# Optimization experiments

Hardware: AMD Instinct MI355X
Metric: run time of the kernel (lower is better)

Reference implementation:

```python
import jax, jax.numpy as jnp
import numpy as np

V0, V1, V2 = 8000, 4000, 4096   # diag / proc / med vocab sizes
E = 512                          # emb_dim
T, L = 64, 48                    # visits, codes per visit
FAI = 0.05                       # history-selection threshold
EPS = 1e-5                       # LayerNorm eps (torch default)

def _normalize(adj):
    # GCN.normalize: row-normalize (adj + I)
    adj = adj + np.eye(adj.shape[0], dtype=np.float64)
    rowsum = adj.sum(1)
    r_inv = np.where(rowsum > 0, 1.0 / rowsum, 0.0)
    return (r_inv[:, None] * adj).astype(np.float32)

def setup_inputs() -> dict:
    key = jax.random.key(0)
    ks = iter(jax.random.split(key, 48))
    p = lambda *s: jax.random.normal(next(ks), s, jnp.float32) * 0.02
    rng = np.random.default_rng(0)
    def rand_adj():
        a = rng.random((V2, V2)) < 0.01
        a = (a | a.T).astype(np.float64)
        np.fill_diagonal(a, 0.0)
        return a
    ehr = rand_adj(); ddi = rand_adj()
    return dict(
        diag_codes=jax.random.randint(next(ks), (T, L), 0, V0),
        proc_codes=jax.random.randint(next(ks), (T, L), 0, V1),
        emb0=p(V0, E), emb1=p(V1, E), emb2=p(V2, E),
        gru1_Wih=p(3 * E, E), gru1_Whh=p(3 * E, E), gru1_bih=p(3 * E), gru1_bhh=p(3 * E),
        gru2_Wih=p(3 * E, E), gru2_Whh=p(3 * E, E), gru2_bih=p(3 * E), gru2_bhh=p(3 * E),
        query_W=p(E, 2 * E), query_b=p(E),
        poly_h1_W=p(32, 2 * E), poly_h1_b=p(32), poly_gate_W=p(1, 32), poly_gate_b=p(1),
        cls_W=p(V2, 2 * E), cls_b=p(V2),
        ln_gamma=jnp.ones((E,), jnp.float32), ln_beta=jnp.zeros((E,), jnp.float32),
        ehr_W1=p(V2, E), ehr_b1=p(E), ehr_W2=p(E, E), ehr_b2=p(E),
        ddi_W1=p(V2, E), ddi_b1=p(E), ddi_W2=p(E, E), ddi_b2=p(E),
        inter1=p(1),
        ehr_adj_norm=jnp.asarray(_normalize(ehr)),
        ddi_adj_norm=jnp.asarray(_normalize(ddi)),
        ddi_adj=jnp.asarray(ddi.astype(np.float32)),
    )

def _gru_last(x_seq, mask, Wih, Whh, bih, bhh):
    # torch nn.GRU cell, batch=1; masked-out steps carry h unchanged, which
    # equals running the GRU over only the selected subsequence. Only the
    # final hidden state is needed (original uses output[-1]).
    def step(h, inp):
        x, m = inp
        gi = x @ Wih.T + bih          # [3E]
        gh = h @ Whh.T + bhh
        ir, iz, inn = jnp.split(gi, 3)
        hr, hz, hn = jnp.split(gh, 3)
        r = jax.nn.sigmoid(ir + hr)
        z = jax.nn.sigmoid(iz + hz)
        n = jnp.tanh(inn + r * hn)
        h_new = (1.0 - z) * n + z * h
        return jnp.where(m, h_new, h), None
    h0 = jnp.zeros((Wih.shape[1],), x_seq.dtype)
    h_final, _ = jax.lax.scan(step, h0, (x_seq, mask))
    return h_final

def reference(diag_codes, proc_codes, emb0, emb1, emb2,
              gru1_Wih, gru1_Whh, gru1_bih, gru1_bhh,
              gru2_Wih, gru2_Whh, gru2_bih, gru2_bhh,
              query_W, query_b, poly_h1_W, poly_h1_b, poly_gate_W, poly_gate_b,
              cls_W, cls_b, ln_gamma, ln_beta,
              ehr_W1, ehr_b1, ehr_W2, ehr_b2, ddi_W1, ddi_b1, ddi_W2, ddi_b2,
              inter1, ehr_adj_norm, ddi_adj_norm, ddi_adj):
    i1 = emb0[diag_codes].sum(1)            # [T,E] per-visit sum pooling
    i2 = emb1[proc_codes].sum(1)            # [T,E]
    rep = jnp.concatenate([i1, i2], -1)     # [T,2E] patient representation
    # Aggregation gate for history selection
    hidden = jax.nn.relu(rep @ poly_h1_W.T + poly_h1_b)
    gate = jax.nn.sigmoid(hidden @ poly_gate_W.T + poly_gate_b)[:, 0]  # [T]
    s = jnp.abs(gate[-1] - gate[:-1])
    mask = jnp.concatenate([s <= FAI, jnp.ones((1,), bool)])  # last visit always kept
    h1 = _gru_last(i1, mask, gru1_Wih, gru1_Whh, gru1_bih, gru1_bhh)
    h2 = _gru_last(i2, mask, gru2_Wih, gru2_Whh, gru2_bih, gru2_bhh)
    q_in = jnp.concatenate([h1, h2])                      # [2E]
    query = (jax.nn.relu(q_in) @ query_W.T + query_b)[None, :]  # [1,E]
    def gcn(W1, b1, W2, b2, adj):
        h = jax.nn.relu(adj @ W1 + b1)    # x = I so x@W1 = W1 (dropout eval)
        return adj @ (h @ W2) + b2
    safe = gcn(ehr_W1, ehr_b1, ehr_W2, ehr_b2, ehr_adj_norm) \
         - inter1 * gcn(ddi_W1, ddi_b1, ddi_W2, ddi_b2, ddi_adj_norm)
    drug = safe + emb2                                    # [V2,E]
    kw = jax.nn.softmax(query @ drug.T, -1)               # [1,V2]
    med = kw @ drug                                       # [1,E]
    mu = query.mean(-1, keepdims=True)
    var = ((query - mu) ** 2).mean(-1, keepdims=True)
    ln = (query - mu) / jnp.sqrt(var + EPS) * ln_gamma + ln_beta
    final = jnp.concatenate([ln, med], -1)                # [1,2E]
    result = jax.nn.relu(final) @ cls_W.T + cls_b         # [1,V2]
    neg = jax.nn.sigmoid(result)
    batch_neg = 0.0005 * ((neg.T * neg) * ddi_adj).sum()
    return result, batch_neg
```

## Files before the change

### kernel.cpp

```cpp
#include <hip/hip_runtime.h>
#include <cstdint>
#include <cstddef>

typedef unsigned short u16;
typedef unsigned int   u32;

typedef __bf16 bf16x8 __attribute__((ext_vector_type(8)));
typedef float  f32x4  __attribute__((ext_vector_type(4)));

__device__ __forceinline__ float uAsF(u32 u){ union{u32 u; float f;} c; c.u=u; return c.f; }
__device__ __forceinline__ float b2f(u16 v){ return uAsF(((u32)v)<<16); }
__device__ __forceinline__ u16 f2b(float f){
  union{float f; u32 u;} c; c.f=f; u32 x=c.u;
  u32 r = (x + 0x7fffu + ((x>>16)&1u)) >> 16;
  return (u16)r;
}
__device__ __forceinline__ void unpack8(uint4 p, float* f){
  f[0]=uAsF(p.x<<16); f[1]=uAsF(p.x&0xffff0000u);
  f[2]=uAsF(p.y<<16); f[3]=uAsF(p.y&0xffff0000u);
  f[4]=uAsF(p.z<<16); f[5]=uAsF(p.z&0xffff0000u);
  f[6]=uAsF(p.w<<16); f[7]=uAsF(p.w&0xffff0000u);
}
__device__ __forceinline__ float sigm(float x){ return 1.f/(1.f+__expf(-x)); }

// ... 180 lines not shown
      og[(size_t)(t0+2)*1536 + j] = a2 + b;
      og[(size_t)(t0+3)*1536 + j] = a3 + b;
      __syncthreads();
      if (tid == 0){
        __threadfence();
        __hip_atomic_fetch_add(&bars[31], 1u, __ATOMIC_RELAXED, __HIP_MEMORY_SCOPE_AGENT);
      }
      return;
    }
    rb -= 96;
    if (rb < 2048 + nt2){
      const void* S = (rb < 2048) ? trS : trS2;
      u16* D = (rb < 2048) ? trD : trD2;
      int t = (rb < 2048) ? rb : rb - 2048;
      __shared__ u16 tile[32][33];
      int bx = t & 15, by = t >> 4;
      int lx = tid & 31, ly = tid >> 5;
      int c = bx*32 + lx;
      #pragma unroll
      for (int i=0;i<2;i++){
        int r = by*32 + ly + i*16;
        size_t idx = (size_t)r*512 + c;
        tile[ly+i*16][lx] = f32 ? f2b(((const float*)S)[idx]) : ((const u16*)S)[idx];
      }
      __syncthreads();
      int r2 = by*32 + lx;
      #pragma unroll
      for (int i=0;i<2;i++){
        int c2 = bx*32 + ly + i*16;
        D[(size_t)c2*4096 + r2] = tile[lx][ly+i*16];
      }
      return;
    }
    rb -= 2048 + nt2;
    if (rb < nc0){
      size_t i8 = ((size_t)rb*512 + tid)*8;
      *(uint4*)(cv0D + i8) = ld8p(cv0S, i8, f32);
      return;
    }
    rb -= nc0;
    if (rb < nc1){
      size_t i8 = ((size_t)rb*512 + tid)*8;
      *(uint4*)(cv1D + i8) = ld8p(cv1S, i8, f32);
      return;
    }
    return;
  }

  const int b = blockIdx.x;
  const int g = b >> 3;
  const int w = b & 7;
  const int e0 = w * 64;
  const void* Whh = g ? Whh1 : Whh0;
  const void* bhh = g ? bhh1 : bhh0;
  const float* gig = gi + (size_t)g*64*1536;

  const int rg = tid & 31;
  const int cg = tid >> 5;

  __shared__ float h_lds[512];
  __shared__ float part[192*17];
  __shared__ float gh_l[192];
  __shared__ float gl[64];
  __shared__ int   mask_l[64];

  u32 wreg[96];
  #pragma unroll
  for (int i=0;i<6;i++){
    int lr = rg*6 + i;
    int grow = (lr >> 6)*512 + e0 + (lr & 63);
    size_t base = (size_t)grow*512 + cg*32;
    if (f32){
      const float2* src = (const float2*)((const float*)Whh + base);
      #pragma unroll
      for (int q=0;q<16;q++){
        float2 v = src[q];
        wreg[i*16+q] = (u32)f2b(v.x) | ((u32)f2b(v.y)<<16);
      }
    } else {
      const uint4* src = (const uint4*)((const u16*)Whh + base);
      #pragma unroll
      for (int q=0;q<4;q++){
        uint4 pk = src[q];
        wreg[i*16+q*4+0]=pk.x; wreg[i*16+q*4+1]=pk.y;
        wreg[i*16+q*4+2]=pk.z; wreg[i*16+q*4+3]=pk.w;
      }
    }
  }
  if (tid < 64) gl[tid] = gate[tid];
  h_lds[tid] = 0.f;
  __syncthreads();
  if (tid < 64)
    mask_l[tid] = (tid==63) ? 1 : (fabsf(gl[63] - gl[tid]) <= 0.05f ? 1 : 0);
  __syncthreads();
  if (tid == 0){
    while (__hip_atomic_load(&bars[31], __ATOMIC_RELAXED, __HIP_MEMORY_SCOPE_AGENT) < 96u)
      __builtin_amdgcn_s_sleep(2);
    __threadfence();
  }
  __syncthreads();

  int s = 0;
  for (int t=0;t<64;t++){
    if (!mask_l[t]) continue;
    s++;
    const int p = s & 1;
    float acc6[6] = {0.f,0.f,0.f,0.f,0.f,0.f};
    const float2* h2 = ((const float2*)h_lds) + cg*16;
    #pragma unroll
    for (int q=0;q<16;q++){
      float2 hv = h2[q];
      #pragma unroll
      for (int i=0;i<6;i++){
        u32 wp = wreg[i*16+q];
        acc6[i] += uAsF(wp<<16)*hv.x + uAsF(wp&0xffff0000u)*hv.y;
      }
    }
    #pragma unroll
    for (int i=0;i<6;i++) part[(rg*6+i)*17 + cg] = acc6[i];
    __syncthreads();
    if (tid < 192){
      const float* pp = part + tid*17;
      float ss = 0.f;
      #pragma unroll
      for (int q=0;q<16;q++) ss += pp[q];
      gh_l[tid] = ss;
    }
    __syncthreads();
    if (tid < 64){
      int e = e0 + tid;
      float hr = gh_l[tid]     + ld1(bhh, e, f32);
      float hz = gh_l[64+tid]  + ld1(bhh, 512+e, f32);
      float hn = gh_l[128+tid] + ld1(bhh, 1024+e, f32);
      const float* git = gig + (size_t)t*1536;
      float ir = git[e], iz = git[512+e], inn = git[1024+e];
      float r = sigm(ir + hr);
      float z = sigm(iz + hz);
      float n = tanhf(inn + r*hn);
      float hnew = (1.f - z)*n + z*h_lds[e];
      u32 word = ((u32)f2b(hnew) << 16) | (u32)s;
      __hip_atomic_store(hbuf + (size_t)p*1024 + g*512 + e, word,
                         __ATOMIC_RELAXED, __HIP_MEMORY_SCOPE_AGENT);
    }
    __syncthreads();
    {
      u32* src = hbuf + (size_t)p*1024 + g*512 + tid;
      u32 word = __hip_atomic_load(src, __ATOMIC_RELAXED, __HIP_MEMORY_SCOPE_AGENT);
      while ((word & 0xffffu) != (u32)s){
        __builtin_amdgcn_s_sleep(1);
        word = __hip_atomic_load(src, __ATOMIC_RELAXED, __HIP_MEMORY_SCOPE_AGENT);
      }
      h_lds[tid] = uAsF(word & 0xffff0000u);
    }
    __syncthreads();
  }
  if (tid < 64) hfin[g*512 + e0 + tid] = h_lds[e0 + tid];
}

__global__ __launch_bounds__(256) void k_transpose(const void* __restrict__ S, u16* __restrict__ D,
                                                   int R, int C, const u16* __restrict__ dt)
{
  int f32 = dprobe(dt);
  __shared__ u16 tile[32][33];
  int lx = threadIdx.x & 31, ly = threadIdx.x >> 5;
  int c = blockIdx.x*32 + lx;
  #pragma unroll
  for (int i=0;i<4;i++){
    int r = blockIdx.y*32 + ly + i*8;
    size_t idx = (size_t)r*C + c;
    tile[ly+i*8][lx] = f32 ? f2b(((const float*)S)[idx]) : ((const u16*)S)[idx];
  }
  __syncthreads();
  int r2 = blockIdx.y*32 + lx;
  #pragma unroll
  for (int i=0;i<4;i++){
    int c2 = blockIdx.x*32 + ly + i*8;
    D[(size_t)c2*R + r2] = tile[lx][ly+i*8];
  }
}

__device__ __forceinline__ void gemm_body(const void* A, const u16* Bt,
    const void* bias, u16* C, int af32, int bf32, int task, u16* As, u16* Bs, int tid)
{
  const int K = 4096;
  const int m0 = (task & 63) * 64;
  const int n0 = (task >> 6) * 128;
  const int lane = tid & 63;
  const int wv = tid >> 6;
  const int wr = wv >> 1, wc = wv & 1;
  const int l15 = lane & 15, lq = lane >> 4;

  f32x4 acc[2][4];
  #pragma unroll
  for (int i=0;i<2;i++)
    #pragma unroll
    for (int j=0;j<4;j++)
      acc[i][j] = (f32x4){0.f,0.f,0.f,0.f};

  const int srow = tid >> 3;
  const int sc8  = tid & 7;
  const size_t grow_a = (size_t)(m0 + srow) * K + sc8*8;
  const size_t grow_b = (size_t)(n0 + srow) * K + sc8*8;
  const int adst0 = srow*64 + ((sc8 ^ (srow&7))*8);
  const int adst1 = (32+srow)*64 + ((sc8 ^ ((32+srow)&7))*8);
  int bdst[4];
  #pragma unroll
  for (int q=0;q<4;q++){
    int row = q*32 + srow;
    bdst[q] = row*64 + ((sc8 ^ (row&7))*8);
  }

  {
    uint4 va0 = ld8p(A, grow_a, af32);
    uint4 va1 = ld8p(A, grow_a + (size_t)32*K, af32);
    uint4 vb[4];
    #pragma unroll
    for (int q=0;q<4;q++) vb[q] = *(const uint4*)(Bt + grow_b + (size_t)q*32*K);
    *(uint4*)(As + adst0) = va0;
    *(uint4*)(As + adst1) = va1;
    #pragma unroll
    for (int q=0;q<4;q++) *(uint4*)(Bs + bdst[q]) = vb[q];
  }
  __syncthreads();

  for (int k0 = 0; k0 < K; k0 += 64){
    const int cur = (k0 >> 6) & 1;
    const int nxt = 1 - cur;
    uint4 va0, va1, vb[4];
    const bool more = (k0 + 64) < K;
    if (more){
      va0 = ld8p(A, grow_a + k0 + 64, af32);
      va1 = ld8p(A, grow_a + (size_t)32*K + k0 + 64, af32);
      #pragma unroll
      for (int q=0;q<4;q++) vb[q] = *(const uint4*)(Bt + grow_b + (size_t)q*32*K + k0 + 64);
    }
    u16* Asc = As + cur*4096;
    u16* Bsc = Bs + cur*8192;
    #pragma unroll
    for (int ks=0; ks<2; ++ks){
      bf16x8 af[2], bfr[4];
      #pragma unroll
      for (int i=0;i<2;i++){
        int ar = wr*32 + i*16 + l15;
        af[i]  = *(const bf16x8*)(Asc + ar*64 + (((ks*4+lq) ^ (ar&7))*8));
      }
      #pragma unroll
      for (int j=0;j<4;j++){
        int br = wc*64 + j*16 + l15;
        bfr[j] = *(const bf16x8*)(Bsc + br*64 + (((ks*4+lq) ^ (br&7))*8));
      }
      #pragma unroll
      for (int i=0;i<2;i++)
        #pragma unroll
        for (int j=0;j<4;j++)
          acc[i][j] = __builtin_amdgcn_mfma_f32_16x16x32_bf16(af[i], bfr[j], acc[i][j], 0,0,0);
    }
    if (more){
      u16* Asn = As + nxt*4096;
      u16* Bsn = Bs + nxt*8192;
      *(uint4*)(Asn + adst0) = va0;
      *(uint4*)(Asn + adst1) = va1;
      #pragma unroll
      for (int q=0;q<4;q++) *(uint4*)(Bsn + bdst[q]) = vb[q];
      __syncthreads();
    }
  }

  #pragma unroll
  for (int i=0;i<2;i++){
    int row = wr*32 + i*16 + lq*4;
    #pragma unroll
    for (int j=0;j<4;j++){
      int col = wc*64 + j*16 + l15;
      int n = n0 + col;
      float bv = ld1(bias, n, bf32);
      #pragma unroll
      for (int r=0;r<4;r++){
        float v = fmaxf(acc[i][j][r] + bv, 0.f);
        C[(size_t)(m0+row+r)*512 + n] = f2b(v);
      }
    }
  }
}

__global__ __launch_bounds__(256)
void k_gemm(const void* __restrict__ A, const u16* __restrict__ Bt,
            const void* __restrict__ bias, u16* __restrict__ C, int K,
            const u16* __restrict__ adt, const u16* __restrict__ bdt)
{
  (void)K;
  __shared__ __attribute__((aligned(16))) char smem[49152];
  int t = (int)blockIdx.x | ((int)blockIdx.y << 6);
  gemm_body(A, Bt, bias, C, dprobe(adt), dprobe(bdt), t, (u16*)smem, (u16*)(smem+16384), threadIdx.x);
}

__global__ __launch_bounds__(256) void k_big(
    const void* __restrict__ Ad, const u16* adt, const u16* __restrict__ W1Td,
    const void* __restrict__ db1, u16* __restrict__ h_d,
    const void* __restrict__ Ae, const u16* aedt, const u16* __restrict__ W1Te,
    const void* __restrict__ eb1, u16* __restrict__ h_,
    const void* __restrict__ E2, const void* __restrict__ W2d, const void* __restrict__ W2e,
    const float* __restrict__ query,
    float* __restrict__ s_emb, float* __restrict__ wv_d, float* __restrict__ wv_e,
    float* __restrict__ zA, float* __restrict__ zB,
    const u16* __restrict__ dt)
{
  __shared__ __attribute__((aligned(16))) char smem[49152];
  const int bid = blockIdx.x, tid = threadIdx.x;
  if (bid < 512){
    if (bid < 256)
      gemm_body(Ad, W1Td, db1, h_d, dprobe(adt), dprobe(dt), bid, (u16*)smem, (u16*)(smem+16384), tid);
    else
      gemm_body(Ae, W1Te, eb1, h_, dprobe(aedt), dprobe(dt), bid-256, (u16*)smem, (u16*)(smem+16384), tid);
    return;
  }
  int t = bid - 512;
  int f32 = dprobe(dt);
  if (t >= 320){
    if (t < 324){
      int rb = t - 320;
      #pragma unroll
      for (int q=0;q<6;q++){ int i = rb*1536 + q*256 + tid; if (i < 6144) zA[i] = 0.f; }
    } else {
      int c = t - 324;
      #pragma unroll
      for (int q=0;q<6;q++){ int i = c*1536 + q*256 + tid; if (i < 4608) zB[i] = 0.f; }
    }
    return;
  }
  float* xl = (float*)smem;
  for (int k=tid; k<512; k+=256) xl[k] = query[k];
  __syncthreads();
  const void* A; float* y; int xb;
  if (t < 256){ A=E2; y=s_emb; xb=t; }
  else if (t < 288){ A=W2d; y=wv_d; xb=t-256; }
  else { A=W2e; y=wv_e; xb=t-288; }
  int w = tid>>6, lane = tid&63;
  int r0 = xb*16 + w*4;
  for (int i=0;i<4;i++){
    int r = r0 + i;
    float s = 0.f;
    int k0 = lane*8;
    float f[8]; ld8(A, (size_t)r*512 + k0, f32, f);
    #pragma unroll
    for (int xx=0;xx<8;xx++) s += f[xx]*xl[k0+xx];
    for (int off=32;off;off>>=1) s += __shfl_down(s, off);
    if (lane==0) y[r] = s;
  }
}

__global__ __launch_bounds__(256) void k_matvec(const void* __restrict__ A, const float* __restrict__ x,
    float* __restrict__ y, int M, int Kc, const u16* __restrict__ dt)
{
  int f32 = dprobe(dt);
  __shared__ float xl[4096];
  int tid = threadIdx.x;
  for (int k=tid; k<Kc; k+=256) xl[k] = x[k];
  __syncthreads();
  int w = tid>>6, lane = tid&63;
  int r0 = blockIdx.x*16 + w*4;
  for (int i=0;i<4;i++){
    int r = r0 + i;
    float s = 0.f;
    for (int k0 = lane*8; k0 < Kc; k0 += 512){
      float f[8]; ld8(A, (size_t)r*Kc + k0, f32, f);
      #pragma unroll
      for (int xx=0;xx<8;xx++) s += f[xx]*xl[k0+xx];
    }
    for (int off=32;off;off>>=1) s += __shfl_down(s, off);
    if (lane==0) y[r] = s;
  }
}

__global__ __launch_bounds__(256) void k_mvp(
    const void* __restrict__ A0, const float* __restrict__ x0, float* __restrict__ y0, const u16* d0,
    const void* __restrict__ A1, const float* __restrict__ x1, float* __restrict__ y1, const u16* d1,
    int Kc, int half)
{
  __shared__ float xl[4096];
  int bx = blockIdx.x, tid = threadIdx.x;
  const void* A; const float* x; float* y; const u16* dtp; int xb;
  if (bx < half){ A=A0; x=x0; y=y0; dtp=d0; xb=bx; }
  else          { A=A1; x=x1; y=y1; dtp=d1; xb=bx-half; }
  int f32 = dprobe(dtp);
  for (int k=tid; k<Kc; k+=256) xl[k] = x[k];
  __syncthreads();
  int w = tid>>6, lane = tid&63;
  int r0 = xb*16 + w*4;
  for (int i=0;i<4;i++){
    int r = r0 + i;
    float s = 0.f;
    for (int k0 = lane*8; k0 < Kc; k0 += 512){
      float f[8]; ld8(A, (size_t)r*Kc + k0, f32, f);
      #pragma unroll
      for (int xx=0;xx<8;xx++) s += f[xx]*xl[k0+xx];
    }
    for (int off=32;off;off>>=1) s += __shfl_down(s, off);
    if (lane==0) y[r] = s;
  }
}

__global__ __launch_bounds__(256) void k_mvps(
    const void* __restrict__ Ae, const float* __restrict__ ue, float* __restrict__ se, const u16* aedt,
    const void* __restrict__ Ad, const float* __restrict__ ud, float* __restrict__ sd, const u16* adt,
    const float* __restrict__ semb, const void* __restrict__ inter1, float* __restrict__ kw,
    u32* __restrict__ tick, const u16* __restrict__ dt)
{
  __shared__ float xl[4096];
  __shared__ int lastf;
  int bx = blockIdx.x, tid = threadIdx.x;
  const void* A; const float* x; float* yy; int f32;
  if (bx < 256){ A=Ae; x=ue; yy=se; f32=dprobe(aedt); }
  else         { A=Ad; x=ud; yy=sd; f32=dprobe(adt); }
  int xb = bx & 255;
  for (int k=tid; k<4096; k+=256) xl[k] = x[k];
  __syncthreads();
  int w = tid>>6, lane = tid&63;
  int r0 = xb*16 + w*4;
  for (int i=0;i<4;i++){
    int r = r0 + i;
    float s = 0.f;
    for (int k0 = lane*8; k0 < 4096; k0 += 512){
      float f[8]; ld8(A, (size_t)r*4096 + k0, f32, f);
      #pragma unroll
      for (int xx=0;xx<8;xx++) s += f[xx]*xl[k0+xx];
    }
    for (int off=32;off;off>>=1) s += __shfl_down(s, off);
    if (lane==0) yy[r] = s;
  }
  __syncthreads();
  if (tid == 0){
    __threadfence();
    u32 old = atomicAdd(tick, 1u);
    lastf = (old == 511u);
    if (lastf) __threadfence();
  }
  __syncthreads();
  if (lastf){
    int df = dprobe(dt);
    float* red = xl;
    float it1 = ld1(inter1, 0, df);
    float v[16]; float m = -1e30f;
    #pragma unroll
    for (int q=0;q<16;q++){
      int i = tid + q*256;
      v[q] = se[i] - it1*sd[i] + semb[i];
      m = fmaxf(m, v[q]);
    }
    red[tid] = m; __syncthreads();
    for (int s=128;s;s>>=1){ if (tid<s) red[tid] = fmaxf(red[tid], red[tid+s]); __syncthreads(); }
    m = red[0]; __syncthreads();
    float sum = 0.f;
    #pragma unroll
    for (int q=0;q<16;q++){ v[q] = __expf(v[q]-m); sum += v[q]; }
    red[tid] = sum; __syncthreads();
    for (int s=128;s;s>>=1){ if (tid<s) red[tid] += red[tid+s]; __syncthreads(); }
    float inv = 1.f/red[0];
    #pragma unroll
    for (int q=0;q<16;q++) kw[tid + q*256] = v[q]*inv;
  }
}

__global__ __launch_bounds__(256) void k_colreduce(const void* __restrict__ A, const float* __restrict__ w,
    float* __restrict__ y, int C, const u16* __restrict__ dt)
{
  int f32 = dprobe(dt);
  __shared__ float wl[256];
  int tid = threadIdx.x;
  int v0 = blockIdx.y*256;
  wl[tid] = w[v0+tid];
  __syncthreads();
  int k = blockIdx.x*256 + tid;
  float acc = 0.f;
  size_t base = (size_t)v0*C + k;
  for (int i=0;i<256;i++) acc += wl[i]*ld1(A, base + (size_t)i*C, f32);
  atomicAdd(&y[k], acc);
}

__global__ __launch_bounds__(256) void k_cr3(
    const void* __restrict__ Ae, const u16* aedt, float* __restrict__ ye,
    const void* __restrict__ Ad, const u16* addt, float* __restrict__ yd,
    const void* __restrict__ E2, const u16* edt, float* __restrict__ ym,
    const float* __restrict__ kw)
{
  __shared__ float wl[256];
  int tid = threadIdx.x, bx = blockIdx.x;
  int v0 = blockIdx.y*256;
  wl[tid] = kw[v0+tid];
  __syncthreads();
  const void* A; float* y; int C, k, f32;
  if (bx < 16){ A=Ae; y=ye; C=4096; k=bx*256+tid; f32=dprobe(aedt); }
  else if (bx < 32){ A=Ad; y=yd; C=4096; k=(bx-16)*256+tid; f32=dprobe(addt); }
  else { A=E2; y=ym; C=512; k=(bx-32)*256+tid; f32=dprobe(edt); }
  float acc = 0.f;
  size_t base = (size_t)v0*C + k;
  for (int i=0;i<256;i++) acc += wl[i]*ld1(A, base + (size_t)i*C, f32);
  atomicAdd(&y[k], acc);
}

__global__ __launch_bounds__(256) void k_crp(
    const void* __restrict__ A0, const float* __restrict__ w0, float* __restrict__ y0, const u16* d0,
    const void* __restrict__ A1, const float* __restrict__ w1, float* __restrict__ y1, const u16* d1,
    int C, int half)
{
  __shared__ float wl[256];
  int tid = threadIdx.x, bx = blockIdx.x;
  int v0 = blockIdx.y*256;
  const void* A; const float* w; float* y; const u16* dtp; int xk;
  if (bx < half){ A=A0; w=w0; y=y0; dtp=d0; xk=bx; }
  else          { A=A1; w=w1; y=y1; dtp=d1; xk=bx-half; }
  int f32 = dprobe(dtp);
  wl[tid] = w[v0+tid];
  __syncthreads();
  int k = xk*256 + tid;
  float acc = 0.f;
  size_t base = (size_t)v0*C + k;
  for (int i=0;i<256;i++) acc += wl[i]*ld1(A, base + (size_t)i*C, f32);
  atomicAdd(&y[k], acc);
}

__global__ __launch_bounds__(256) void k_crpln(
    const void* __restrict__ eW2, const float* __restrict__ z, float* __restrict__ me,
    const void* __restrict__ dW2, const float* __restrict__ z2, float* __restrict__ mdp,
    const float* __restrict__ query, const float* __restrict__ memb,
    const void* __restrict__ eb2, const void* __restrict__ db2, const void* __restrict__ inter1,
    const void* __restrict__ gam, const void* __restrict__ bet,
    float* __restrict__ fin, u32* __restrict__ tick, const u16* __restrict__ dt)
{
  __shared__ float wl[256];
  __shared__ int lastf;
  int tid = threadIdx.x, bx = blockIdx.x;
  int f32 = dprobe(dt);
  {
    int side = bx >> 2;
    int sub  = bx & 3;
    int xk = sub & 1;
    int v0 = (sub >> 1) * 256;
    const void* A = side ? dW2 : eW2;
    const float* w = side ? z2 : z;
    float* y = side ? mdp : me;
    wl[tid] = w[v0+tid];
    __syncthreads();
    int k = xk*256 + tid;
    float acc = 0.f;
    size_t base = (size_t)v0*512 + k;
    for (int i=0;i<256;i++) acc += wl[i]*ld1(A, base + (size_t)i*512, f32);
    atomicAdd(&y[k], acc);
  }
  __syncthreads();
  if (tid == 0){
    __threadfence();
    u32 old = atomicAdd(tick, 1u);
    lastf = (old == 7u);
    if (lastf) __threadfence();
  }
  __syncthreads();
  if (lastf){
    float* red = wl;
    float q0 = query[tid], q1 = query[tid+256];
    red[tid] = q0 + q1; __syncthreads();
    for (int s=128;s;s>>=1){ if (tid<s) red[tid] += red[tid+s]; __syncthreads(); }
    float mu = red[0]/512.f; __syncthreads();
    float d0 = q0 - mu, d1 = q1 - mu;
    red[tid] = d0*d0 + d1*d1; __syncthreads();
    for (int s=128;s;s>>=1){ if (tid<s) red[tid] += red[tid+s]; __syncthreads(); }
    float rstd = rsqrtf(red[0]/512.f + 1e-5f);
    float it1 = ld1(inter1, 0, f32);
    int e0 = tid, e1 = tid + 256;
    float ln0 = d0*rstd*ld1(gam,e0,f32) + ld1(bet,e0,f32);
    float ln1 = d1*rstd*ld1(gam,e1,f32) + ld1(bet,e1,f32);
    float mv0 = (me[e0] + ld1(eb2,e0,f32)) - it1*(mdp[e0] + ld1(db2,e0,f32)) + memb[e0];
    float mv1 = (me[e1] + ld1(eb2,e1,f32)) - it1*(mdp[e1] + ld1(db2,e1,f32)) + memb[e1];
    fin[e0] = fmaxf(ln0, 0.f);
    fin[e1] = fmaxf(ln1, 0.f);
    fin[512+e0] = fmaxf(mv0, 0.f);
    fin[512+e1] = fmaxf(mv1, 0.f);
  }
}

__global__ void k_zero(float* __restrict__ p, int n){
  int i = blockIdx.x*1024 + threadIdx.x;
  if (i < n) p[i] = 0.f;
}

__global__ __launch_bounds__(256) void k_mv3(
    const void* __restrict__ E2, const void* __restrict__ W2d, const void* __restrict__ W2e,
    const float* __restrict__ query,
    float* __restrict__ s_emb, float* __restrict__ wv_d, float* __restrict__ wv_e,
    float* __restrict__ zA, float* __restrict__ zB, float* __restrict__ nega,
    u32* __restrict__ ctr, const u16* __restrict__ dt)
{
  int bx = blockIdx.x, tid = threadIdx.x;
  if (bx >= 320){
    int rb = bx - 320;
    if (rb < 4){
      #pragma unroll
      for (int q=0;q<6;q++){ int i = rb*1536 + q*256 + tid; if (i < 6144) zA[i] = 0.f; }
    } else if (rb < 7){
      int c = rb - 4;
      #pragma unroll
      for (int q=0;q<6;q++){ int i = c*1536 + q*256 + tid; if (i < 4608) zB[i] = 0.f; }
    } else if (tid == 0){
      *nega = 0.f; ctr[0] = 0u; ctr[1] = 0u;
    }
    return;
  }
  int f32 = dprobe(dt);
  __shared__ float xl[512];
  for (int k=tid; k<512; k+=256) xl[k] = query[k];
  __syncthreads();
  const void* A; float* y; int xb;
  if (bx < 256){ A=E2; y=s_emb; xb=bx; }
  else if (bx < 288){ A=W2d; y=wv_d; xb=bx-256; }
  else { A=W2e; y=wv_e; xb=bx-288; }
  int w = tid>>6, lane = tid&63;
  int r0 = xb*16 + w*4;
  for (int i=0;i<4;i++){
    int r = r0 + i;
    float s = 0.f;
    {
      int k0 = lane*8;
      float f[8]; ld8(A, (size_t)r*512 + k0, f32, f);
      #pragma unroll
      for (int xx=0;xx<8;xx++) s += f[xx]*xl[k0+xx];
    }
    for (int off=32;off;off>>=1) s += __shfl_down(s, off);
    if (lane==0) y[r] = s;
  }
}

__global__ __launch_bounds__(256) void k_query(const float* __restrict__ hfin,
    const void* __restrict__ qW, const void* __restrict__ qb,
    float* __restrict__ query, const u16* __restrict__ dt)
{
  int f32 = dprobe(dt);
  __shared__ float qin[1024];
  int tid = threadIdx.x;
  for (int q=0;q<4;q++){ int k=tid+q*256; qin[k] = fmaxf(hfin[k], 0.f); }
  __syncthreads();
  int w = tid>>6, lane = tid&63;
  int row0 = blockIdx.x*64 + w*16;
  for (int i=0;i<16;i++){
    int rr = row0 + i;
    float s = 0.f;
    for (int k=lane;k<1024;k+=64) s += qin[k]*ld1(qW, (size_t)rr*1024+k, f32);
    for (int off=32;off;off>>=1) s += __shfl_down(s, off);
    if (lane==0) query[rr] = s + ld1(qb, rr, f32);
  }
}

__global__ __launch_bounds__(1024) void k_softmax(const float* __restrict__ se, const float* __restrict__ sd,
    const float* __restrict__ semb, const void* __restrict__ inter1,
    float* __restrict__ kw, const u16* __restrict__ dt)
{
  int f32 = dprobe(dt);
  __shared__ float red[1024];
  int tid = threadIdx.x;
  float it1 = ld1(inter1, 0, f32);
  float v[4]; float m = -1e30f;
  for (int q=0;q<4;q++){
    int i = tid + q*1024;
    v[q] = se[i] - it1*sd[i] + semb[i];
    m = fmaxf(m, v[q]);
  }
  red[tid] = m; __syncthreads();
  for (int s=512;s;s>>=1){ if (tid<s) red[tid] = fmaxf(red[tid], red[tid+s]); __syncthreads(); }
  m = red[0]; __syncthreads();
  float sum = 0.f;
  for (int q=0;q<4;q++){ v[q] = __expf(v[q]-m); sum += v[q]; }
  red[tid] = sum; __syncthreads();
  for (int s=512;s;s>>=1){ if (tid<s) red[tid] += red[tid+s]; __syncthreads(); }
  float inv = 1.f/red[0];
  for (int q=0;q<4;q++) kw[tid + q*1024] = v[q]*inv;
}

__global__ __launch_bounds__(512) void k_ln(const float* __restrict__ query,
    const float* __restrict__ me, const float* __restrict__ md, const float* __restrict__ memb,
    const void* __restrict__ eb2, const void* __restrict__ db2, const void* __restrict__ inter1,
    const void* __restrict__ gam, const void* __restrict__ bet,
    float* __restrict__ fin, const u16* __restrict__ dt)
{
  int f32 = dprobe(dt);
  __shared__ float red[512];
  int tid = threadIdx.x;
  float q = query[tid];
  red[tid] = q; __syncthreads();
  for (int s=256;s;s>>=1){ if (tid<s) red[tid] += red[tid+s]; __syncthreads(); }
  float mu = red[0]/512.f; __syncthreads();
  float d = q - mu;
  red[tid] = d*d; __syncthreads();
  for (int s=256;s;s>>=1){ if (tid<s) red[tid] += red[tid+s]; __syncthreads(); }
  float var = red[0]/512.f;
  float ln = d * rsqrtf(var + 1e-5f) * ld1(gam, tid, f32) + ld1(bet, tid, f32);
  float it1 = ld1(inter1, 0, f32);
  float med = (me[tid] + ld1(eb2, tid, f32)) - it1*(md[tid] + ld1(db2, tid, f32)) + memb[tid];
  fin[tid]      = fmaxf(ln, 0.f);
  fin[512+tid]  = fmaxf(med, 0.f);
}

__global__ __launch_bounds__(256) void k_cls(const float* __restrict__ fin,
    const void* __restrict__ clsW, const void* __restrict__ clsb,
    void* __restrict__ outv, float* __restrict__ neg, const u16* __restrict__ dt)
{
  int f32 = dprobe(dt);
  __shared__ float fl[1024];
  int tid = threadIdx.x;
  for (int q=0;q<4;q++) fl[tid+q*256] = fin[tid+q*256];
  __syncthreads();
  int w = tid>>6, lane = tid&63;
  int v0 = blockIdx.x*64 + w*16;
  for (int i=0;i<16;i++){
    int v = v0+i;
    float f[16];
    ld8(clsW, (size_t)v*1024 + lane*16, f32, f);
    ld8(clsW, (size_t)v*1024 + lane*16 + 8, f32, f+8);
    const float* q16 = fl + lane*16;
    float s = 0.f;
    #pragma unroll
    for (int x=0;x<16;x++) s += f[x]*q16[x];
    for (int off=32;off;off>>=1) s += __shfl_down(s, off);
    if (lane==0){
      s += ld1(clsb, v, f32);
      if (f32) ((float*)outv)[v] = s; else ((u16*)outv)[v] = f2b(s);
      neg[v] = sigm(s);
    }
  }
}

__global__ __launch_bounds__(256) void k_negsum(const void* __restrict__ ddi,
    const float* __restrict__ neg, float* __restrict__ acc,
    u32* __restrict__ ctr, void* __restrict__ outv, const u16* __restrict__ dt)
{
  int f32 = dprobe(dt);
  __shared__ float nl[4096];
  int tid = threadIdx.x;
  for (int q=0;q<16;q++) nl[tid+q*256] = neg[tid+q*256];
  __syncthreads();
  int w = tid>>6, lane = tid&63;
  int i0 = blockIdx.x*32 + w*8;
  float tot = 0.f;
  for (int i=0;i<8;i++){
    int ii = i0+i;
    size_t base = (size_t)ii*4096;
    float s = 0.f;
    for (int step=0; step<16; step++){
      int k = lane*4 + step*256;
      float f[4]; ld4(ddi, base + k, f32, f);
      s += f[0]*nl[k] + f[1]*nl[k+1] + f[2]*nl[k+2] + f[3]*nl[k+3];
    }
    for (int off=32;off;off>>=1) s += __shfl_down(s, off);
    if (lane==0) tot += nl[ii]*s;
  }
  if (lane==0) atomicAdd(acc, tot);
  __syncthreads();
  if (tid == 0){
    __threadfence();
    u32 old = atomicAdd(ctr, 1u);
    if (old == (u32)(gridDim.x - 1)){
      float v = 0.0005f * __hip_atomic_load(acc, __ATOMIC_RELAXED, __HIP_MEMORY_SCOPE_AGENT);
      if (f32) ((float*)outv)[4096] = v; else ((u16*)outv)[4096] = f2b(v);
    }
  }
}

__global__ void k_diag(u16* __restrict__ outv, float dv)
{
  int i = blockIdx.x*256 + threadIdx.x;
  if (i <= 4096) outv[i] = (i==0) ? f2b(dv) : (u16)0;
}

extern "C" void kernel_launch(void* const* d_in, const int* in_sizes, int n_in,
                              void* d_out, int out_size, void* d_ws, size_t ws_size,
                              hipStream_t stream)
{
  (void)in_sizes; (void)n_in; (void)out_size;
  const int* diag = (const int*)d_in[0];
  const int* proc = (const int*)d_in[1];
  const void* emb0 = d_in[2];
  const void* emb1 = d_in[3];
  const void* emb2 = d_in[4];
  const void* g1Wih=d_in[5];  const void* g1Whh=d_in[6];
  const void* g1bih=d_in[7];  const void* g1bhh=d_in[8];
  const void* g2Wih=d_in[9];  const void* g2Whh=d_in[10];
  const void* g2bih=d_in[11]; const void* g2bhh=d_in[12];
  const void* qW =d_in[13];   const void* qb =d_in[14];
  const void* phW=d_in[15];   const void* phb=d_in[16];
  const void* pgW=d_in[17];   const void* pgb=d_in[18];
  const void* clsW=d_in[19];  const void* clsb=d_in[20];
  const void* lng=d_in[21];   const void* lnb=d_in[22];
  const void* eW1=d_in[23];   const void* eb1=d_in[24];
  const void* eW2=d_in[25];   const void* eb2=d_in[26];
  const void* dW1=d_in[27];   const void* db1=d_in[28];
  const void* dW2=d_in[29];   const void* db2=d_in[30];
  const void* inter1=d_in[31];
  const void* eAdj=d_in[32];
  const void* dAdjN=d_in[33];
  const void* dAdj=d_in[34];

  const u16* dt = (const u16*)lng;

  if (ws_size < NEED_C){
    unsigned mb = (unsigned)(ws_size >> 20);
    int b = 0;
    while ((2u << b) <= mb + 1 && b < 15) b++;
    k_diag<<<17, 256, 0, stream>>>((u16*)d_out, 30000.f + 1000.f*(float)b);
    return;
  }

  const bool hasHd  = ws_size >= NEED_C2;
  const bool hasAb  = ws_size >= NEED_B;
  const bool hasAb2 = ws_size >= NEED_A;
  const bool hasW2  = ws_size >= NEED_A2;
  const bool mergedTail = hasHd && (hasAb2 || !hasAb);

  char* ws = (char*)d_ws;
  float* i1    = (float*)(ws + OFF_I1);
  float* i2    = (float*)(ws + OFF_I2);
  float* gi    = (float*)(ws + OFF_GI);
  float* gate  = (float*)(ws + OFF_GATE);
  u32*   hbuf  = (u32*)  (ws + OFF_HBUF);
  float* hfin  = (float*)(ws + OFF_HFIN);
  u32*   ctr   = (u32*)  (ws + OFF_CTR);
  float* nega  = (float*)(ws + OFF_NEGA);
  u32*   bars  = (u32*)  (ws + OFF_BAR);
  float* query = (float*)(ws + OFF_QUERY);
  float* s_e   = (float*)(ws + OFF_SE);
  float* s_d   = (float*)(ws + OFF_SD);
  float* s_emb = (float*)(ws + OFF_SEMB);
  float* kw    = (float*)(ws + OFF_KW);
  float* u_e   = (float*)(ws + OFF_U);
  float* y     = (float*)(ws + OFF_Y);
  float* z     = (float*)(ws + OFF_Z);
  float* me    = (float*)(ws + OFF_ME);
  float* md    = (float*)(ws + OFF_MD);
  float* memb  = (float*)(ws + OFF_MEMB);
  float* fin   = (float*)(ws + OFF_FIN);
  float* neg   = (float*)(ws + OFF_NEG);
  u16*   W1T   = (u16*)  (ws + OFF_W1T);
  u16*   W1TE  = (u16*)  (ws + OFF_W1TE);
  u16*   h     = (u16*)  (ws + OFF_H);
  u16*   h_d   = hasHd ? (u16*)(ws + OFF_HD) : h;
  u16*   AbD   = (u16*)  (ws + OFF_ABD);
  u16*   AbE   = hasAb2 ? (u16*)(ws + OFF_ABE) : AbD;
  float* u_d   = (float*)(ws + OFF_UD);
  float* y2    = (float*)(ws + OFF_Y2);
  float* z2    = (float*)(ws + OFF_Z2);
  float* wv_d  = (float*)(ws + OFF_WVD);
  float* wv_e  = (float*)(ws + OFF_WVE);
  void*  outv  = d_out;

  const void* Ad   = hasAb ? (const void*)AbD : dAdjN;
  const u16*  adt  = hasAb ? (const u16*)nullptr : dt;
  const void* Ae   = hasAb ? (const void*)AbE : eAdj;
  const u16*  aedt = hasAb ? (const u16*)nullptr : dt;

  k_gg<<<65, 256, 0, stream>>>(diag, proc, emb0, emb1, phW, phb, pgW, pgb,
                               i1, i2, gate, bars, nega, ctr, dt);

  {
    int nt2 = hasW2 ? 2048 : 0;
    int nc0 = hasAb  ? 4096 : 0;
    int nc1 = hasAb2 ? 4096 : 0;
    k_gruf2<<<16 + 96 + 2048 + nt2 + nc0 + nc1, 512, 0, stream>>>(
        g1Whh, g2Whh, g1bhh, g2bhh,
        g1Wih, g2Wih, g1bih, g2bih,
        i1, i2, gi, gate, hbuf, hfin, bars, dt,
        dW1, W1T,
        eW1, W1TE, nt2,
        dAdjN, AbD, nc0,
        eAdj,  AbE, nc1);
  }

  if (mergedTail){
    k_query<<<8, 256, 0, stream>>>(hfin, qW, qb, query, dt);
    if (hasW2){
      k_big<<<839, 256, 0, stream>>>(Ad, adt, W1T, db1, h_d,
                                     Ae, aedt, W1TE, eb1, h,
                                     emb2, dW2, eW2, query,
                                     s_emb, wv_d, wv_e, y, y2, dt);
    } else {
      k_mv3<<<328, 256, 0, stream>>>(emb2, dW2, eW2, query, s_emb, wv_d, wv_e,
                                     y, y2, nega, ctr, dt);
      k_gemm<<<dim3(64,4), 256, 0, stream>>>(Ad, W1T, db1, h_d, 4096, adt, dt);
      k_transpose<<<dim3(16,128), 256, 0, stream>>>(eW1, W1T, 4096, 512, dt);
      k_gemm<<<dim3(64,4), 256, 0, stream>>>(Ae, W1T, eb1, h, 4096, aedt, dt);
    }
    k_mvp<<<512, 256, 0, stream>>>(h, wv_e, u_e, nullptr, h_d, wv_d, u_d, nullptr, 512, 256);
    k_mvps<<<512, 256, 0, stream>>>(Ae, u_e, s_e, aedt, Ad, u_d, s_d, adt,
                                    s_emb, inter1, kw, &bars[29], dt);
    k_cr3<<<dim3(34,16), 256, 0, stream>>>(Ae, aedt, y, Ad, adt, y2, emb2, dt, memb, kw);
    k_crp<<<dim3(4,16), 256, 0, stream>>>(h, y, z, nullptr, h_d, y2, z2, nullptr, 512, 2);
    k_crpln<<<8, 256, 0, stream>>>(eW2, z, me, dW2, z2, md,
                                   query, memb, eb2, db2, inter1, lng, lnb,
                                   fin, &bars[28], dt);
    k_cls<<<64, 256, 0, stream>>>(fin, clsW, clsb, outv, neg, dt);
    k_negsum<<<128, 256, 0, stream>>>(dAdj, neg, nega, ctr, outv, dt);
  } else {
    k_query<<<8, 256, 0, stream>>>(hfin, qW, qb, query, dt);
    k_mv3<<<328, 256, 0, stream>>>(emb2, dW2, eW2, query, s_emb, wv_d, wv_e,
                                   y, y2, nega, ctr, dt);
    k_gemm<<<dim3(64,4), 256, 0, stream>>>(Ad, W1T, db1, h_d, 4096, adt, dt);
    k_matvec<<<256, 256, 0, stream>>>(h_d, wv_d, u_e, 4096, 512, nullptr);
    k_matvec<<<256, 256, 0, stream>>>(Ad, u_e, s_d, 4096, 4096, adt);

    if (hasAb) k_cvt<<<8192, 256, 0, stream>>>(eAdj, AbE, dt);
    k_transpose<<<dim3(16,128), 256, 0, stream>>>(eW1, W1T, 4096, 512, dt);
    k_gemm<<<dim3(64,4), 256, 0, stream>>>(Ae, W1T, eb1, h, 4096, aedt, dt);
    k_matvec<<<256, 256, 0, stream>>>(h, wv_e, u_e, 4096, 512, nullptr);
    k_matvec<<<256, 256, 0, stream>>>(Ae, u_e, s_e, 4096, 4096, aedt);

    k_softmax<<<1, 1024, 0, stream>>>(s_e, s_d, s_emb, inter1, kw, dt);

    k_colreduce<<<dim3(16,16), 256, 0, stream>>>(Ae, kw, y, 4096, aedt);
    k_colreduce<<<dim3(2,16),  256, 0, stream>>>(h,  y,  z, 512,  nullptr);
    k_colreduce<<<dim3(2,2),   256, 0, stream>>>(eW2, z, me, 512, dt);
    k_colreduce<<<dim3(2,16),  256, 0, stream>>>(emb2, kw, memb, 512, dt);

    k_zero<<<5, 1024, 0, stream>>>(y, 4608);
    if (hasAb && !hasAb2) k_cvt<<<8192, 256, 0, stream>>>(dAdjN, AbD, dt);
    if (!hasHd){
      k_transpose<<<dim3(16,128), 256, 0, stream>>>(dW1, W1T, 4096, 512, dt);
      k_gemm<<<dim3(64,4), 256, 0, stream>>>(Ad, W1T, db1, h, 4096, adt, dt);
    }
    k_colreduce<<<dim3(16,16), 256, 0, stream>>>(Ad, kw, y, 4096, adt);
    k_colreduce<<<dim3(2,16),  256, 0, stream>>>(h_d, y, z, 512, nullptr);
    k_colreduce<<<dim3(2,2),   256, 0, stream>>>(dW2, z, md, 512, dt);

    k_ln<<<1, 512, 0, stream>>>(query, me, md, memb, eb2, db2, inter1, lng, lnb, fin, dt);
    k_cls<<<64, 256, 0, stream>>>(fin, clsW, clsb, outv, neg, dt);
    k_negsum<<<128, 256, 0, stream>>>(dAdj, neg, nega, ctr, outv, dt);
  }
}
```

Measured before the change: 1.029 ms.

## Split tail matvecs and column reductions into finer, vectorized blocks

In the merged tail, the adjacency-vector products now split K into four chunks across 2048 blocks and accumulate with atomics; k_big also zeroes the s_e accumulator. The column reductions over adjacency, emb2 and GCN hidden states change to 64-row tiles with 8-wide vector loads per thread. The classifier and negative-sum kernels get finer row partitioning over more blocks. This raises parallelism and memory-level concurrency in the bandwidth-bound tail, at the cost of more atomics and nondeterministic summation order.

Result: faster. 1.008 ms (-2.0%).

```diff
diff --git a/kernel.cpp b/kernel.cpp
--- a/kernel.cpp
+++ b/kernel.cpp
@@ -506,7 +506,7 @@
     const void* __restrict__ E2, const void* __restrict__ W2d, const void* __restrict__ W2e,
     const float* __restrict__ query,
     float* __restrict__ s_emb, float* __restrict__ wv_d, float* __restrict__ wv_e,
-    float* __restrict__ zA, float* __restrict__ zB,
+    float* __restrict__ zA, float* __restrict__ zB, float* __restrict__ zC,
     const u16* __restrict__ dt)
 {
   __shared__ __attribute__((aligned(16))) char smem[49152];
@@ -525,10 +525,14 @@
       int rb = t - 320;
       #pragma unroll
       for (int q=0;q<6;q++){ int i = rb*1536 + q*256 + tid; if (i < 6144) zA[i] = 0.f; }
+    } else if (t < 327){
+      int c = t - 324;
+      #pragma unroll
+      for (int q=0;q<6;q++){ int i = c*1536 + q*256 + tid; if (i < 4608) zB[i] = 0.f; }
     } else {
-      int c = t - 324;
-      #pragma unroll
-      for (int q=0;q<6;q++){ int i = c*1536 + q*256 + tid; if (i < 4608) zB[i] = 0.f; }
+      int c = t - 327;
+      #pragma unroll
+      for (int q=0;q<6;q++){ int i = c*1536 + q*256 + tid; if (i < 8192) zC[i] = 0.f; }
     }
     return;
   }
@@ -604,6 +608,70 @@
   }
 }
 
+__global__ __launch_bounds__(256) void k_mvps2(
+    const void* __restrict__ Ae, const float* __restrict__ ue, float* __restrict__ se, const u16* aedt,
+    const void* __restrict__ Ad, const float* __restrict__ ud, float* __restrict__ sd, const u16* adt,
+    const float* __restrict__ semb, const void* __restrict__ inter1, float* __restrict__ kw,
+    u32* __restrict__ tick, const u16* __restrict__ dt)
+{
+  __shared__ float xl[1024];
+  __shared__ int lastf;
+  int bx = blockIdx.x, tid = threadIdx.x;
+  const void* A; const float* x; float* yy; int f32;
+  if (bx < 1024){ A=Ae; x=ue; yy=se; f32=dprobe(aedt); }
+  else          { A=Ad; x=ud; yy=sd; f32=dprobe(adt); }
+  int r = bx & 1023;
+  int xb = r >> 2, kc = r & 3;
+  for (int k=tid; k<1024; k+=256) xl[k] = x[kc*1024 + k];
+  __syncthreads();
+  int w = tid>>6, lane = tid&63;
+  int r0 = xb*16 + w*4;
+  for (int i=0;i<4;i++){
+    int rr = r0 + i;
+    float s = 0.f;
+    #pragma unroll
+    for (int step=0; step<2; step++){
+      int k0 = lane*8 + step*512;
+      float f[8]; ld8(A, (size_t)rr*4096 + kc*1024 + k0, f32, f);
+      #pragma unroll
+      for (int xx=0;xx<8;xx++) s += f[xx]*xl[k0+xx];
+    }
+    for (int off=32;off;off>>=1) s += __shfl_down(s, off);
+    if (lane==0) atomicAdd(&yy[rr], s);
+  }
+  __syncthreads();
+  if (tid == 0){
+    __threadfence();
+    u32 old = atomicAdd(tick, 1u);
+    lastf = (old == 2047u);
+    if (lastf) __threadfence();
+  }
+  __syncthreads();
+  if (lastf){
+    int df = dprobe(dt);
+    float* red = xl;
+    float it1 = ld1(inter1, 0, df);
+    float v[16]; float m = -1e30f;
+    #pragma unroll
+    for (int q=0;q<16;q++){
+      int i = tid + q*256;
+      v[q] = se[i] - it1*sd[i] + semb[i];
+      m = fmaxf(m, v[q]);
+    }
+    red[tid] = m; __syncthreads();
+    for (int s=128;s;s>>=1){ if (tid<s) red[tid] = fmaxf(red[tid], red[tid+s]); __syncthreads(); }
+    m = red[0]; __syncthreads();
+    float sum = 0.f;
+    #pragma unroll
+    for (int q=0;q<16;q++){ v[q] = __expf(v[q]-m); sum += v[q]; }
+    red[tid] = sum; __syncthreads();
+    for (int s=128;s;s>>=1){ if (tid<s) red[tid] += red[tid+s]; __syncthreads(); }
+    float inv = 1.f/red[0];
+    #pragma unroll
+    for (int q=0;q<16;q++) kw[tid + q*256] = v[q]*inv;
+  }
+}
+
 __global__ __launch_bounds__(256) void k_mvps(
     const void* __restrict__ Ae, const float* __restrict__ ue, float* __restrict__ se, const u16* aedt,
     const void* __restrict__ Ad, const float* __restrict__ ud, float* __restrict__ sd, const u16* adt,
@@ -681,46 +749,57 @@
   atomicAdd(&y[k], acc);
 }
 
-__global__ __launch_bounds__(256) void k_cr3(
+__global__ __launch_bounds__(256) void k_cr3v(
     const void* __restrict__ Ae, const u16* aedt, float* __restrict__ ye,
     const void* __restrict__ Ad, const u16* addt, float* __restrict__ yd,
     const void* __restrict__ E2, const u16* edt, float* __restrict__ ym,
     const float* __restrict__ kw)
 {
-  __shared__ float wl[256];
-  int tid = threadIdx.x, bx = blockIdx.x;
-  int v0 = blockIdx.y*256;
-  wl[tid] = kw[v0+tid];
-  __syncthreads();
-  const void* A; float* y; int C, k, f32;
-  if (bx < 16){ A=Ae; y=ye; C=4096; k=bx*256+tid; f32=dprobe(aedt); }
-  else if (bx < 32){ A=Ad; y=yd; C=4096; k=(bx-16)*256+tid; f32=dprobe(addt); }
-  else { A=E2; y=ym; C=512; k=(bx-32)*256+tid; f32=dprobe(edt); }
-  float acc = 0.f;
-  size_t base = (size_t)v0*C + k;
-  for (int i=0;i<256;i++) acc += wl[i]*ld1(A, base + (size_t)i*C, f32);
-  atomicAdd(&y[k], acc);
-}
-
-__global__ __launch_bounds__(256) void k_crp(
-    const void* __restrict__ A0, const float* __restrict__ w0, float* __restrict__ y0, const u16* d0,
-    const void* __restrict__ A1, const float* __restrict__ w1, float* __restrict__ y1, const u16* d1,
-    int C, int half)
-{
-  __shared__ float wl[256];
-  int tid = threadIdx.x, bx = blockIdx.x;
-  int v0 = blockIdx.y*256;
-  const void* A; const float* w; float* y; const u16* dtp; int xk;
-  if (bx < half){ A=A0; w=w0; y=y0; dtp=d0; xk=bx; }
-  else          { A=A1; w=w1; y=y1; dtp=d1; xk=bx-half; }
-  int f32 = dprobe(dtp);
-  wl[tid] = w[v0+tid];
-  __syncthreads();
-  int k = xk*256 + tid;
-  float acc = 0.f;
-  size_t base = (size_t)v0*C + k;
-  for (int i=0;i<256;i++) acc += wl[i]*ld1(A, base + (size_t)i*C, f32);
-  atomicAdd(&y[k], acc);
+  __shared__ float wl[64];
+  int tid = threadIdx.x, gx = blockIdx.x, gy = blockIdx.y;
+  int v0 = gy*64;
+  if (tid < 64) wl[tid] = kw[v0+tid];
+  __syncthreads();
+  const void* A; float* y; int C, c0, f32;
+  if (gx < 2){ A=Ae; y=ye; C=4096; c0=gx*2048; f32=dprobe(aedt); }
+  else if (gx < 4){ A=Ad; y=yd; C=4096; c0=(gx-2)*2048; f32=dprobe(addt); }
+  else { A=E2; y=ym; C=512; c0=0; f32=dprobe(edt); if (tid >= 64) return; }
+  int c = c0 + tid*8;
+  float acc[8] = {0.f,0.f,0.f,0.f,0.f,0.f,0.f,0.f};
+  for (int i=0;i<64;i++){
+    float f[8]; ld8(A, (size_t)(v0+i)*C + c, f32, f);
+    float wv = wl[i];
+    #pragma unroll
+    for (int j=0;j<8;j++) acc[j] += wv*f[j];
+  }
+  #pragma unroll
+  for (int j=0;j<8;j++) atomicAdd(&y[c+j], acc[j]);
+}
+
+__global__ __launch_bounds__(256) void k_crpv(
+    const u16* __restrict__ A0, const float* __restrict__ w0, float* __restrict__ y0,
+    const u16* __restrict__ A1, const float* __restrict__ w1, float* __restrict__ y1)
+{
+  __shared__ float wl[64];
+  int tid = threadIdx.x, gx = blockIdx.x, gy = blockIdx.y;
+  int v0 = gy*64;
+  const u16* A = gx ? A1 : A0;
+  const float* w = gx ? w1 : w0;
+  float* y = gx ? y1 : y0;
+  if (tid < 64) wl[tid] = w[v0+tid];
+  __syncthreads();
+  int sub = tid>>6, lane = tid&63;
+  int c = lane*8;
+  float acc[8] = {0.f,0.f,0.f,0.f,0.f,0.f,0.f,0.f};
+  for (int i=sub*16; i<sub*16+16; i++){
+    float f[8];
+    unpack8(*(const uint4*)(A + (size_t)(v0+i)*512 + c), f);
+    float wv = wl[i];
+    #pragma unroll
+    for (int j=0;j<8;j++) acc[j] += wv*f[j];
+  }
+  #pragma unroll
+  for (int j=0;j<8;j++) atomicAdd(&y[c+j], acc[j]);
 }
 
 __global__ __launch_bounds__(256) void k_crpln(
@@ -931,6 +1010,35 @@
   }
 }
 
+__global__ __launch_bounds__(256) void k_clsv(const float* __restrict__ fin,
+    const void* __restrict__ clsW, const void* __restrict__ clsb,
+    void* __restrict__ outv, float* __restrict__ neg, const u16* __restrict__ dt)
+{
+  int f32 = dprobe(dt);
+  __shared__ float fl[1024];
+  int tid = threadIdx.x;
+  for (int q=0;q<4;q++) fl[tid+q*256] = fin[tid+q*256];
+  __syncthreads();
+  int w = tid>>6, lane = tid&63;
+  int v0 = blockIdx.x*16 + w*4;
+  for (int i=0;i<4;i++){
+    int v = v0+i;
+    float f[16];
+    ld8(clsW, (size_t)v*1024 + lane*16, f32, f);
+    ld8(clsW, (size_t)v*1024 + lane*16 + 8, f32, f+8);
+    const float* q16 = fl + lane*16;
+    float s = 0.f;
+    #pragma unroll
+    for (int x=0;x<16;x++) s += f[x]*q16[x];
+    for (int off=32;off;off>>=1) s += __shfl_down(s, off);
+    if (lane==0){
+      s += ld1(clsb, v, f32);
+      if (f32) ((float*)outv)[v] = s; else ((u16*)outv)[v] = f2b(s);
+      neg[v] = sigm(s);
+    }
+  }
+}
+
 __global__ __launch_bounds__(256) void k_negsum(const void* __restrict__ ddi,
     const float* __restrict__ neg, float* __restrict__ acc,
     u32* __restrict__ ctr, void* __restrict__ outv, const u16* __restrict__ dt)
@@ -944,6 +1052,42 @@
   int i0 = blockIdx.x*32 + w*8;
   float tot = 0.f;
   for (int i=0;i<8;i++){
+    int ii = i0+i;
+    size_t base = (size_t)ii*4096;
+    float s = 0.f;
+    for (int step=0; step<16; step++){
+      int k = lane*4 + step*256;
+      float f[4]; ld4(ddi, base + k, f32, f);
+      s += f[0]*nl[k] + f[1]*nl[k+1] + f[2]*nl[k+2] + f[3]*nl[k+3];
+    }
+    for (int off=32;off;off>>=1) s += __shfl_down(s, off);
+    if (lane==0) tot += nl[ii]*s;
+  }
+  if (lane==0) atomicAdd(acc, tot);
+  __syncthreads();
+  if (tid == 0){
+    __threadfence();
+    u32 old = atomicAdd(ctr, 1u);
+    if (old == (u32)(gridDim.x - 1)){
+      float v = 0.0005f * __hip_atomic_load(acc, __ATOMIC_RELAXED, __HIP_MEMORY_SCOPE_AGENT);
+      if (f32) ((float*)outv)[4096] = v; else ((u16*)outv)[4096] = f2b(v);
+    }
+  }
+}
+
+__global__ __launch_bounds__(256) void k_negsumv(const void* __restrict__ ddi,
+    const float* __restrict__ neg, float* __restrict__ acc,
+    u32* __restrict__ ctr, void* __restrict__ outv, const u16* __restrict__ dt)
+{
+  int f32 = dprobe(dt);
+  __shared__ float nl[4096];
+  int tid = threadIdx.x;
+  for (int q=0;q<16;q++) nl[tid+q*256] = neg[tid+q*256];
+  __syncthreads();
+  int w = tid>>6, lane = tid&63;
+  int i0 = blockIdx.x*16 + w*4;
+  float tot = 0.f;
+  for (int i=0;i<4;i++){
     int ii = i0+i;
     size_t base = (size_t)ii*4096;
     float s = 0.f;
@@ -1075,25 +1219,37 @@
         eAdj,  AbE, nc1);
   }
 
-  if (mergedTail){
+  if (mergedTail && hasW2){
     k_query<<<8, 256, 0, stream>>>(hfin, qW, qb, query, dt);
-    if (hasW2){
-      k_big<<<839, 256, 0, stream>>>(Ad, adt, W1T, db1, h_d,
-                                     Ae, aedt, W1TE, eb1, h,
-                                     emb2, dW2, eW2, query,
-                                     s_emb, wv_d, wv_e, y, y2, dt);
-    } else {
-      k_mv3<<<328, 256, 0, stream>>>(emb2, dW2, eW2, query, s_emb, wv_d, wv_e,
-                                     y, y2, nega, ctr, dt);
-      k_gemm<<<dim3(64,4), 256, 0, stream>>>(Ad, W1T, db1, h_d, 4096, adt, dt);
-      k_transpose<<<dim3(16,128), 256, 0, stream>>>(eW1, W1T, 4096, 512, dt);
-      k_gemm<<<dim3(64,4), 256, 0, stream>>>(Ae, W1T, eb1, h, 4096, aedt, dt);
-    }
+    k_big<<<845, 256, 0, stream>>>(Ad, adt, W1T, db1, h_d,
+                                   Ae, aedt, W1TE, eb1, h,
+                                   emb2, dW2, eW2, query,
+                                   s_emb, wv_d, wv_e, y, y2, s_e, dt);
+    k_mvp<<<512, 256, 0, stream>>>(h, wv_e, u_e, nullptr, h_d, wv_d, u_d, nullptr, 512, 256);
+    k_mvps2<<<2048, 256, 0, stream>>>(Ae, u_e, s_e, aedt, Ad, u_d, s_d, adt,
+                                      s_emb, inter1, kw, &bars[29], dt);
+    k_cr3v<<<dim3(5,64), 256, 0, stream>>>(Ae, aedt, y, Ad, adt, y2, emb2, dt, memb, kw);
+    k_crpv<<<dim3(2,64), 256, 0, stream>>>(h, y, z, h_d, y2, z2);
+    k_crpln<<<8, 256, 0, stream>>>(eW2, z, me, dW2, z2, md,
+                                   query, memb, eb2, db2, inter1, lng, lnb,
+                                   fin, &bars[28], dt);
+    k_clsv<<<256, 256, 0, stream>>>(fin, clsW, clsb, outv, neg, dt);
+    k_negsumv<<<256, 256, 0, stream>>>(dAdj, neg, nega, ctr, outv, dt);
+  } else if (mergedTail){
+    k_query<<<8, 256, 0, stream>>>(hfin, qW, qb, query, dt);
+    k_mv3<<<328, 256, 0, stream>>>(emb2, dW2, eW2, query, s_emb, wv_d, wv_e,
+                                   y, y2, nega, ctr, dt);
+    k_gemm<<<dim3(64,4), 256, 0, stream>>>(Ad, W1T, db1, h_d, 4096, adt, dt);
+    k_transpose<<<dim3(16,128), 256, 0, stream>>>(eW1, W1T, 4096, 512, dt);
+    k_gemm<<<dim3(64,4), 256, 0, stream>>>(Ae, W1T, eb1, h, 4096, aedt, dt);
     k_mvp<<<512, 256, 0, stream>>>(h, wv_e, u_e, nullptr, h_d, wv_d, u_d, nullptr, 512, 256);
     k_mvps<<<512, 256, 0, stream>>>(Ae, u_e, s_e, aedt, Ad, u_d, s_d, adt,
                                     s_emb, inter1, kw, &bars[29], dt);
-    k_cr3<<<dim3(34,16), 256, 0, stream>>>(Ae, aedt, y, Ad, adt, y2, emb2, dt, memb, kw);
-    k_crp<<<dim3(4,16), 256, 0, stream>>>(h, y, z, nullptr, h_d, y2, z2, nullptr, 512, 2);
+    k_colreduce<<<dim3(16,16), 256, 0, stream>>>(Ae, kw, y, 4096, aedt);
+    k_colreduce<<<dim3(16,16), 256, 0, stream>>>(Ad, kw, y2, 4096, adt);
+    k_colreduce<<<dim3(2,16),  256, 0, stream>>>(emb2, kw, memb, 512, dt);
+    k_colreduce<<<dim3(2,16),  256, 0, stream>>>(h,  y,  z, 512,  nullptr);
+    k_colreduce<<<dim3(2,16),  256, 0, stream>>>(h_d, y2, z2, 512, nullptr);
     k_crpln<<<8, 256, 0, stream>>>(eW2, z, me, dW2, z2, md,
                                    query, memb, eb2, db2, inter1, lng, lnb,
                                    fin, &bars[28], dt);
```
